# Kernel optimization log

Hardware: AMD Instinct MI355X
Metric: run time of the kernel (lower is better)

## Reference

```python
import jax, jax.numpy as jnp
import numpy as np

B, N, F, P = 8, 16384, 128, 28


def setup_inputs() -> dict:
    key = jax.random.key(0)
    k1, k2 = jax.random.split(key)
    x = jax.random.uniform(k1, (B, N, 2), dtype=jnp.float32)  # 2D coords in [0,1]
    sigma = jnp.full((1,), np.log(0.05), dtype=jnp.float32)   # learned log-lengthscale
    image_features = jax.random.normal(k2, (F, P, P), dtype=jnp.float32) / np.sqrt(F)
    return {"x": x, "sigma": sigma, "image_features": image_features}


def reference(x, sigma, image_features):
    # x: [B, N, 2], sigma: [1] (log lengthscale), image_features: [F, P, P]
    P_ = image_features.shape[-1]
    grid = jnp.linspace(0.001, 1.0 - 0.001, P_, dtype=x.dtype)  # [P]
    ls = jnp.exp(sigma[0])                                      # lengthscale
    inv = 0.5 / (ls * ls)
    # pairwise squared dists grid vs each coordinate axis -> [B, P, N]
    d0 = (grid[None, :, None] - x[:, None, :, 0]) ** 2
    d1 = (grid[None, :, None] - x[:, None, :, 1]) ** 2
    k0 = jnp.exp(-inv * d0)  # [B, P, N]
    k1 = jnp.exp(-inv * d1)  # [B, P, N]
    # features[b,n,f] = sum_{p,q} k0[b,p,n] * IF[f,p,q] * k1[b,q,n]
    feats = jnp.einsum('bpn,fpq,bqn->bnf', k0, image_features, k1)
    return feats
```

## Files before the change

kernel.cpp:

```cpp
#include <hip/hip_runtime.h>

#define FDIM  128
#define PDIM  28
#define KPAD  896
#define MPTS  131072

typedef _Float16 half8   __attribute__((ext_vector_type(8)));
typedef _Float16 half4v  __attribute__((ext_vector_type(4)));
typedef float    floatx4 __attribute__((ext_vector_type(4)));

__global__ __launch_bounds__(256) void prep_ift(const float* __restrict__ IF,
                                                _Float16* __restrict__ IFt) {
    int idx = blockIdx.x * 256 + threadIdx.x;
    int f = idx / KPAD;
    int k = idx - f * KPAD;
    int p = k >> 5;
    int q = k & 31;
    float v = (q < PDIM) ? IF[f * (PDIM * PDIM) + p * PDIM + q] : 0.0f;
    IFt[idx] = (_Float16)v;
}

__global__ __launch_bounds__(256, 3) void feats_kernel(
    const float* __restrict__ x,
    const float* __restrict__ sigma,
    const _Float16* __restrict__ IFt,
    float* __restrict__ out)
{
    __shared__ _Float16               k0s[128 * 36];
    __shared__ __align__(16) _Float16 k1s[128 * 40];

    const int tid  = threadIdx.x;
    const int lane = tid & 63;
    const int wave = tid >> 6;
    const int ln15 = lane & 15;
    const int quad = lane >> 4;

    const float ls    = __expf(sigma[0]);
    const float inv   = 0.5f / (ls * ls);
    const float gstep = 0.998f / 27.0f;

    {
        const int ptl = tid & 127;
        const int ptg = blockIdx.x * 128 + ptl;
        if (tid < 128) {
            const float x0 = x[2 * ptg + 0];
            #pragma unroll
            for (int p = 0; p < PDIM; p++) {
                float d = (0.001f + p * gstep) - x0;
                k0s[ptl * 36 + p] = (_Float16)__expf(-inv * d * d);
            }
        } else {
            const float x1 = x[2 * ptg + 1];
            #pragma unroll
            for (int q = 0; q < PDIM; q++) {
                float d = (0.001f + q * gstep) - x1;
                k1s[ptl * 40 + q] = (_Float16)__expf(-inv * d * d);
            }
            #pragma unroll
            for (int q = PDIM; q < 32; q++)
                k1s[ptl * 40 + q] = (_Float16)0.0f;
        }
    }
    __syncthreads();

    half8 k1f[8];
    #pragma unroll
    for (int mt = 0; mt < 8; mt++) {
        const int m = mt * 16 + ln15;
        k1f[mt] = *(const half8*)&k1s[m * 40 + quad * 8];
    }

    floatx4 acc[8][2];
    #pragma unroll
    for (int mt = 0; mt < 8; mt++) {
        acc[mt][0] = (floatx4){0.0f, 0.0f, 0.0f, 0.0f};
        acc[mt][1] = (floatx4){0.0f, 0.0f, 0.0f, 0.0f};
    }

    const _Float16* gB0 = IFt + (size_t)(wave * 32 + ln15) * KPAD + quad * 8;
    const _Float16* gB1 = gB0 + 16 * KPAD;

    #define KSTEP(J)                                                          \
    {                                                                         \
        half8 bf0 = *(const half8*)(gB0 + kk4 * 128 + (J) * 32);              \
        half8 bf1 = *(const half8*)(gB1 + kk4 * 128 + (J) * 32);              \
        _Pragma("unroll")                                                     \
        for (int mt = 0; mt < 8; mt++) {                                      \
            const half8 af = k1f[mt] * k0v[mt][(J)];                          \
            acc[mt][0] = __builtin_amdgcn_mfma_f32_16x16x32_f16(              \
                af, bf0, acc[mt][0], 0, 0, 0);                                \
            acc[mt][1] = __builtin_amdgcn_mfma_f32_16x16x32_f16(              \
                af, bf1, acc[mt][1], 0, 0, 0);                                \
        }                                                                     \
    }

    #pragma unroll 1
    for (int kk4 = 0; kk4 < 7; kk4++) {
        half4v k0v[8];
        #pragma unroll
        for (int mt = 0; mt < 8; mt++) {
            const int m = mt * 16 + ln15;
            k0v[mt] = *(const half4v*)&k0s[m * 36 + kk4 * 4];
        }
        KSTEP(0)
        KSTEP(1)
        KSTEP(2)
        KSTEP(3)
    }
    #undef KSTEP

    #pragma unroll
    for (int mt = 0; mt < 8; mt++) {
        const int row0 = blockIdx.x * 128 + mt * 16 + quad * 4;
        #pragma unroll
        for (int nt = 0; nt < 2; nt++) {
            const int col = wave * 32 + nt * 16 + ln15;
            float* op = out + (size_t)row0 * FDIM + col;
            #pragma unroll
            for (int r = 0; r < 4; r++)
                __builtin_nontemporal_store(acc[mt][nt][r], op + (size_t)r * FDIM);
        }
    }
}

extern "C" void kernel_launch(void* const* d_in, const int* in_sizes, int n_in,
                              void* d_out, int out_size, void* d_ws, size_t ws_size,
                              hipStream_t stream) {
    const float* x     = (const float*)d_in[0];
    const float* sigma = (const float*)d_in[1];
    const float* IF    = (const float*)d_in[2];
    float* out = (float*)d_out;

    _Float16* IFt = (_Float16*)d_ws;

    prep_ift<<<(FDIM * KPAD) / 256, 256, 0, stream>>>(IF, IFt);
    feats_kernel<<<MPTS / 128, 256, 0, stream>>>(x, sigma, IFt, out);
}
```

Before: 108.6 us.

## Stage IF operand tiles through double-buffered LDS with register prefetch

The B operand (fp16 image features) is no longer read directly from global memory by each wave. Each k-step's slice is now loaded cooperatively into a double-buffered shared-memory tile, and the next slice is prefetched into registers while the MFMAs run. Global loads get coalesced and shared across waves. In exchange there is a __syncthreads per k-step (27 barriers) and more LDS use, which may lower occupancy below the 3 blocks per CU requested.

```diff
diff --git a/kernel.cpp b/kernel.cpp
--- a/kernel.cpp
+++ b/kernel.cpp
@@ -28,6 +28,7 @@
 {
     __shared__ _Float16               k0s[128 * 36];
     __shared__ __align__(16) _Float16 k1s[128 * 40];
+    __shared__ __align__(16) _Float16 bs[2][128 * 40];
 
     const int tid  = threadIdx.x;
     const int lane = tid & 63;
@@ -38,6 +39,20 @@
     const float ls    = __expf(sigma[0]);
     const float inv   = 0.5f / (ls * ls);
     const float gstep = 0.998f / 27.0f;
+
+    const uint4* gI = (const uint4*)IFt;
+    const int c0 = tid, c1 = tid + 256;
+    const int f0 = c0 >> 2, cq0 = c0 & 3;
+    const int f1 = c1 >> 2, cq1 = c1 & 3;
+    const int bo0 = f0 * 40 + cq0 * 8;
+    const int bo1 = f1 * 40 + cq1 * 8;
+
+    {
+        uint4 p0 = gI[f0 * 112 + cq0];
+        uint4 p1 = gI[f1 * 112 + cq1];
+        *(uint4*)&bs[0][bo0] = p0;
+        *(uint4*)&bs[0][bo1] = p1;
+    }
 
     {
         const int ptl = tid & 127;
@@ -65,10 +80,8 @@
 
     half8 k1f[8];
     #pragma unroll
-    for (int mt = 0; mt < 8; mt++) {
-        const int m = mt * 16 + ln15;
-        k1f[mt] = *(const half8*)&k1s[m * 40 + quad * 8];
-    }
+    for (int mt = 0; mt < 8; mt++)
+        k1f[mt] = *(const half8*)&k1s[(mt * 16 + ln15) * 40 + quad * 8];
 
     floatx4 acc[8][2];
     #pragma unroll
@@ -77,13 +90,20 @@
         acc[mt][1] = (floatx4){0.0f, 0.0f, 0.0f, 0.0f};
     }
 
-    const _Float16* gB0 = IFt + (size_t)(wave * 32 + ln15) * KPAD + quad * 8;
-    const _Float16* gB1 = gB0 + 16 * KPAD;
+    const int nrow0 = (wave * 32 + ln15) * 40 + quad * 8;
+    const int nrow1 = (wave * 32 + 16 + ln15) * 40 + quad * 8;
 
     #define KSTEP(J)                                                          \
     {                                                                         \
-        half8 bf0 = *(const half8*)(gB0 + kk4 * 128 + (J) * 32);              \
-        half8 bf1 = *(const half8*)(gB1 + kk4 * 128 + (J) * 32);              \
+        const int kk = kk4 * 4 + (J);                                         \
+        uint4 p0, p1;                                                         \
+        if (kk < PDIM - 1) {                                                  \
+            p0 = gI[f0 * 112 + (kk + 1) * 4 + cq0];                           \
+            p1 = gI[f1 * 112 + (kk + 1) * 4 + cq1];                           \
+        }                                                                     \
+        const _Float16* buf = bs[kk & 1];                                     \
+        half8 bf0 = *(const half8*)&buf[nrow0];                               \
+        half8 bf1 = *(const half8*)&buf[nrow1];                               \
         _Pragma("unroll")                                                     \
         for (int mt = 0; mt < 8; mt++) {                                      \
             const half8 af = k1f[mt] * k0v[mt][(J)];                          \
@@ -92,16 +112,20 @@
             acc[mt][1] = __builtin_amdgcn_mfma_f32_16x16x32_f16(              \
                 af, bf1, acc[mt][1], 0, 0, 0);                                \
         }                                                                     \
+        if (kk < PDIM - 1) {                                                  \
+            _Float16* nbuf = (_Float16*)bs[(kk + 1) & 1];                     \
+            *(uint4*)&nbuf[bo0] = p0;                                         \
+            *(uint4*)&nbuf[bo1] = p1;                                         \
+            __syncthreads();                                                  \
+        }                                                                     \
     }
 
     #pragma unroll 1
     for (int kk4 = 0; kk4 < 7; kk4++) {
         half4v k0v[8];
         #pragma unroll
-        for (int mt = 0; mt < 8; mt++) {
-            const int m = mt * 16 + ln15;
-            k0v[mt] = *(const half4v*)&k0s[m * 36 + kk4 * 4];
-        }
+        for (int mt = 0; mt < 8; mt++)
+            k0v[mt] = *(const half4v*)&k0s[(mt * 16 + ln15) * 36 + kk4 * 4];
         KSTEP(0)
         KSTEP(1)
         KSTEP(2)
```

New measurement: 132.1 us. 21.6% more time.

## Stage half of IF in LDS per persistent block and loop over point chunks

Applied to the files above, without the earlier changes.

Each block now loads a 64-feature slice of the fp16 image-feature matrix into padded shared memory once, then loops over 8 chunks of 128 points, recomputing the Gaussian factors per chunk and feeding MFMA B operands from LDS instead of global memory. The grid shrinks to 256 persistent blocks, with feature halves split across block pairs. This removes repeated global/L2 reads of the B matrix, at the cost of duplicated exp work across the two feature halves, lower occupancy (~115KB LDS, launch bound 1), and extra barriers per chunk.

```diff
diff --git a/kernel.cpp b/kernel.cpp
--- a/kernel.cpp
+++ b/kernel.cpp
@@ -4,6 +4,7 @@
 #define PDIM  28
 #define KPAD  896
 #define MPTS  131072
+#define BSTR  904
 
 typedef _Float16 half8   __attribute__((ext_vector_type(8)));
 typedef _Float16 half4v  __attribute__((ext_vector_type(4)));
@@ -20,12 +21,13 @@
     IFt[idx] = (_Float16)v;
 }
 
-__global__ __launch_bounds__(256, 3) void feats_kernel(
+__global__ __launch_bounds__(256, 1) void feats_kernel(
     const float* __restrict__ x,
     const float* __restrict__ sigma,
     const _Float16* __restrict__ IFt,
     float* __restrict__ out)
 {
+    __shared__ __align__(16) _Float16 bs[64 * BSTR];
     __shared__ _Float16               k0s[128 * 36];
     __shared__ __align__(16) _Float16 k1s[128 * 40];
 
@@ -35,90 +37,92 @@
     const int ln15 = lane & 15;
     const int quad = lane >> 4;
 
+    const int fs    = blockIdx.x & 1;
+    const int mg    = blockIdx.x >> 1;
+    const int fbase = fs * 64;
+
     const float ls    = __expf(sigma[0]);
     const float inv   = 0.5f / (ls * ls);
     const float gstep = 0.998f / 27.0f;
 
     {
-        const int ptl = tid & 127;
-        const int ptg = blockIdx.x * 128 + ptl;
-        if (tid < 128) {
-            const float x0 = x[2 * ptg + 0];
-            #pragma unroll
-            for (int p = 0; p < PDIM; p++) {
-                float d = (0.001f + p * gstep) - x0;
-                k0s[ptl * 36 + p] = (_Float16)__expf(-inv * d * d);
-            }
-        } else {
-            const float x1 = x[2 * ptg + 1];
-            #pragma unroll
-            for (int q = 0; q < PDIM; q++) {
-                float d = (0.001f + q * gstep) - x1;
-                k1s[ptl * 40 + q] = (_Float16)__expf(-inv * d * d);
-            }
-            #pragma unroll
-            for (int q = PDIM; q < 32; q++)
-                k1s[ptl * 40 + q] = (_Float16)0.0f;
-        }
-    }
-    __syncthreads();
-
-    half8 k1f[8];
-    #pragma unroll
-    for (int mt = 0; mt < 8; mt++) {
-        const int m = mt * 16 + ln15;
-        k1f[mt] = *(const half8*)&k1s[m * 40 + quad * 8];
+        const int row = tid >> 2;
+        const int qtr = tid & 3;
+        const uint4* g = (const uint4*)(IFt + (size_t)(fbase + row) * KPAD) + qtr * 28;
+        uint4* l = (uint4*)&bs[row * BSTR] + qtr * 28;
+        #pragma unroll
+        for (int j = 0; j < 28; j++)
+            l[j] = g[j];
     }
 
-    floatx4 acc[8][2];
-    #pragma unroll
-    for (int mt = 0; mt < 8; mt++) {
-        acc[mt][0] = (floatx4){0.0f, 0.0f, 0.0f, 0.0f};
-        acc[mt][1] = (floatx4){0.0f, 0.0f, 0.0f, 0.0f};
-    }
-
-    const _Float16* gB0 = IFt + (size_t)(wave * 32 + ln15) * KPAD + quad * 8;
-    const _Float16* gB1 = gB0 + 16 * KPAD;
-
-    #define KSTEP(J)                                                          \
-    {                                                                         \
-        half8 bf0 = *(const half8*)(gB0 + kk4 * 128 + (J) * 32);              \
-        half8 bf1 = *(const half8*)(gB1 + kk4 * 128 + (J) * 32);              \
-        _Pragma("unroll")                                                     \
-        for (int mt = 0; mt < 8; mt++) {                                      \
-            const half8 af = k1f[mt] * k0v[mt][(J)];                          \
-            acc[mt][0] = __builtin_amdgcn_mfma_f32_16x16x32_f16(              \
-                af, bf0, acc[mt][0], 0, 0, 0);                                \
-            acc[mt][1] = __builtin_amdgcn_mfma_f32_16x16x32_f16(              \
-                af, bf1, acc[mt][1], 0, 0, 0);                                \
-        }                                                                     \
-    }
+    const int bfo = (wave * 16 + ln15) * BSTR + quad * 8;
 
     #pragma unroll 1
-    for (int kk4 = 0; kk4 < 7; kk4++) {
-        half4v k0v[8];
+    for (int c = 0; c < 8; c++) {
+        const int chunkbase = mg * 1024 + c * 128;
+
+        __syncthreads();
+
+        {
+            const int ptl = tid & 127;
+            const int ptg = chunkbase + ptl;
+            if (tid < 128) {
+                const float x0 = x[2 * ptg + 0];
+                #pragma unroll
+                for (int p = 0; p < PDIM; p++) {
+                    float d = (0.001f + p * gstep) - x0;
+                    k0s[ptl * 36 + p] = (_Float16)__expf(-inv * d * d);
+                }
+            } else {
+                const float x1 = x[2 * ptg + 1];
+                #pragma unroll
+                for (int q = 0; q < PDIM; q++) {
+                    float d = (0.001f + q * gstep) - x1;
+                    k1s[ptl * 40 + q] = (_Float16)__expf(-inv * d * d);
+                }
+                #pragma unroll
+                for (int q = PDIM; q < 32; q++)
+                    k1s[ptl * 40 + q] = (_Float16)0.0f;
+            }
+        }
+        __syncthreads();
+
+        half8 k1f[8];
+        #pragma unroll
+        for (int mt = 0; mt < 8; mt++)
+            k1f[mt] = *(const half8*)&k1s[(mt * 16 + ln15) * 40 + quad * 8];
+
+        floatx4 acc[8];
+        #pragma unroll
+        for (int mt = 0; mt < 8; mt++)
+            acc[mt] = (floatx4){0.0f, 0.0f, 0.0f, 0.0f};
+
+        #pragma unroll 1
+        for (int kk4 = 0; kk4 < 7; kk4++) {
+            half4v k0v[8];
+            #pragma unroll
+            for (int mt = 0; mt < 8; mt++)
+                k0v[mt] = *(const half4v*)&k0s[(mt * 16 + ln15) * 36 + kk4 * 4];
+            #pragma unroll
+            for (int j = 0; j < 4; j++) {
+                const half8 bf = *(const half8*)&bs[bfo + (kk4 * 4 + j) * 32];
+                #pragma unroll
+                for (int mt = 0; mt < 8; mt++) {
+                    const half8 af = k1f[mt] * k0v[mt][j];
+                    acc[mt] = __builtin_amdgcn_mfma_f32_16x16x32_f16(
+                        af, bf, acc[mt], 0, 0, 0);
+                }
+            }
+        }
+
+        const int col = fbase + wave * 16 + ln15;
         #pragma unroll
         for (int mt = 0; mt < 8; mt++) {
-            const int m = mt * 16 + ln15;
-            k0v[mt] = *(const half4v*)&k0s[m * 36 + kk4 * 4];
-        }
-        KSTEP(0)
-        KSTEP(1)
-        KSTEP(2)
-        KSTEP(3)
-    }
-    #undef KSTEP
-
-    #pragma unroll
-    for (int mt = 0; mt < 8; mt++) {
-        const int row0 = blockIdx.x * 128 + mt * 16 + quad * 4;
-        #pragma unroll
-        for (int nt = 0; nt < 2; nt++) {
-            const int col = wave * 32 + nt * 16 + ln15;
+            const int row0 = chunkbase + mt * 16 + quad * 4;
             float* op = out + (size_t)row0 * FDIM + col;
             #pragma unroll
             for (int r = 0; r < 4; r++)
-                __builtin_nontemporal_store(acc[mt][nt][r], op + (size_t)r * FDIM);
+                __builtin_nontemporal_store(acc[mt][r], op + (size_t)r * FDIM);
         }
     }
 }
@@ -134,5 +138,5 @@
     _Float16* IFt = (_Float16*)d_ws;
 
     prep_ift<<<(FDIM * KPAD) / 256, 256, 0, stream>>>(IF, IFt);
-    feats_kernel<<<MPTS / 128, 256, 0, stream>>>(x, sigma, IFt, out);
+    feats_kernel<<<256, 256, 0, stream>>>(x, sigma, IFt, out);
 }
```

After: 116.0 us. +6.8%, slower.
